# Kernel optimization log

Hardware: AMD Instinct MI355X
Metric: run time of the kernel (lower is better)

## Reference

```python
import jax, jax.numpy as jnp
import numpy as np

H, DH = 8, 64
DIM = 512
INNER = H * DH
GAMMA = 0.01
LAMBDA_REG = 0.001


def _ln(x, g, b, eps=1e-5):
    mu = x.mean(-1, keepdims=True)
    var = x.var(-1, keepdims=True)  # ddof=0, matches torch LayerNorm
    return (x - mu) / jnp.sqrt(var + eps) * g + b


def _proj(x, ln_g, ln_b, W):
    # LayerNorm -> Linear(no bias) -> split heads: [Q,N,DIM] -> [H,Q,N,DH]
    Q, N, _ = x.shape
    y = _ln(x, ln_g, ln_b) @ W
    return jnp.transpose(y.reshape(Q, N, H, DH), (2, 0, 1, 3))


def setup_inputs() -> dict:
    key = jax.random.key(0)
    ks = jax.random.split(key, 10)
    s = 0.02
    return {
        "q": jax.random.normal(ks[0], (16, 512, DIM), jnp.float32),
        "k": jax.random.normal(ks[1], (16, 512, DIM), jnp.float32),
        "v": jax.random.normal(ks[2], (16, 512, DIM), jnp.float32),
        "ln_g": jnp.ones((DIM,), jnp.float32),
        "ln_b": jnp.zeros((DIM,), jnp.float32),
        "W_in": jax.random.normal(ks[3], (DIM, INNER), jnp.float32) * s,
        "wp1_w": jax.random.normal(ks[4], (2 * DH, DH), jnp.float32) * s,
        "wp1_b": jnp.zeros((DH,), jnp.float32),
        "wpln_g": jnp.ones((DH,), jnp.float32),
        "wpln_b": jnp.zeros((DH,), jnp.float32),
        "wp2_w": jax.random.normal(ks[5], (DH, DH // 2), jnp.float32) * s,
        "wp2_b": jnp.zeros((DH // 2,), jnp.float32),
        "wp3_w": jax.random.normal(ks[6], (DH // 2, 3), jnp.float32) * s,
        "wp3_b": jnp.zeros((3,), jnp.float32),
        "temp": jnp.ones((1,), jnp.float32) * 5.0,
        "W_out": jax.random.normal(ks[7], (INNER, DIM), jnp.float32) * s,
        "b_out": jnp.zeros((DIM,), jnp.float32),
    }


def reference(q, k, v, ln_g, ln_b, W_in, wp1_w, wp1_b, wpln_g, wpln_b,
              wp2_w, wp2_b, wp3_w, wp3_b, temp, W_out, b_out):
    sg = jax.lax.stop_gradient
    std1 = lambda x: jnp.std(x, ddof=1)  # torch.std is unbiased

    f_q = _proj(q, ln_g, ln_b, W_in)  # [H,Q,N,DH]
    f_k = _proj(k, ln_g, ln_b, W_in)  # [H,Q,M,DH]
    f_v = _proj(v, ln_g, ln_b, W_in)
    m = f_k.shape[2]

    # --- cosine similarity component (cosine_distance + extra clamp) ---
    dots_raw = jnp.einsum('hqnd,hqmd->hqnm', f_q, f_k)
    n1 = jnp.linalg.norm(f_q, axis=-1, keepdims=True) + 1e-8          # [H,Q,N,1]
    n2 = jnp.linalg.norm(f_k, axis=-1, keepdims=True) + 1e-8          # [H,Q,M,1]
    cosine_sim = jnp.clip(dots_raw / (n1 * jnp.swapaxes(n2, -1, -2)), -0.99, 0.99)

    # --- regularized covariance component ---
    f_kc = f_k - f_k.mean(axis=2, keepdims=True)
    f_qc = f_q - f_q.mean(axis=-1, keepdims=True)
    cov = jnp.einsum('hqnd,hqmd->hqnm', f_qc, f_kc) / (DH ** 0.5 + 1e-8)
    cov = jnp.clip((LAMBDA_REG / max(m, 1)) * cov, -10.0, 10.0)

    # --- margin-based variance component (eval mode: adaptive_gamma == GAMMA) ---
    fqn = f_q / jnp.maximum(jnp.linalg.norm(f_q, axis=-1, keepdims=True), 1e-8)
    fkn = f_k / jnp.maximum(jnp.linalg.norm(f_k, axis=-1, keepdims=True), 1e-8)
    cs = jnp.clip(jnp.einsum('hqnd,hqmd->hqnm', fqn, fkn), -0.99, 0.99)
    margin = jnp.clip(GAMMA - cs, 0.0, 2.0)
    var_comp = jnp.broadcast_to(margin.mean(-1, keepdims=True), cs.shape)

    # --- dynamic weight predictor (dropouts identity in eval) ---
    qg = f_q.mean(axis=(1, 2))                 # [H,DH]
    kg = f_k.mean(axis=(1, 2))
    feats = jnp.concatenate([qg, kg], axis=-1)  # [H,2*DH]
    h1 = jax.nn.relu(_ln(feats @ wp1_w + wp1_b, wpln_g, wpln_b))
    h2 = jax.nn.relu(h1 @ wp2_w + wp2_b)
    logits = jax.nn.softmax(h2 @ wp3_w + wp3_b, axis=-1)  # softmax inside Sequential
    weights = jax.nn.softmax(logits / jnp.clip(temp, 0.1, 20.0), axis=-1)  # [H,3]
    cos_w = weights[:, 0].reshape(H, 1, 1, 1)
    cov_w = weights[:, 1].reshape(H, 1, 1, 1)
    var_w = weights[:, 2].reshape(H, 1, 1, 1)

    # --- global-std rescale + mix + adaptive temperature ---
    cos_s = cosine_sim / (sg(std1(cosine_sim)) + 1e-8)
    cov_s = cov / (sg(std1(cov)) + 1e-8) * 0.1
    var_s = var_comp / (sg(std1(var_comp)) + 1e-8) * 0.1
    dots = cos_w * cos_s + cov_w * cov_s + var_w * var_s
    attn_t = 1.0 + 0.5 * sg(std1(dots))
    dots = dots / jnp.clip(attn_t, 0.5, 5.0)

    out = jnp.einsum('hqnm,hqmd->hqnd', jax.nn.softmax(dots, axis=-1), f_v)
    out = jnp.transpose(out, (1, 2, 0, 3)).reshape(q.shape[0], q.shape[1], INNER)
    return out @ W_out + b_out
```

## Files before the change

kernel.cpp:

```cpp
#include <hip/hip_runtime.h>
#include <math.h>

#define NH 8
#define DHD 64
#define DMODEL 512
#define QB 16
#define SEQ 512
#define NROWS (QB*SEQ)
#define NHQ (NH*QB)
#define KCOV ((float)((0.001/512.0)/(8.0+1e-8)))

typedef __attribute__((ext_vector_type(8))) short short8;
typedef __attribute__((ext_vector_type(8))) unsigned short ushort8v;
typedef __attribute__((ext_vector_type(4))) unsigned short ushort4v;
typedef __attribute__((ext_vector_type(4))) float f32x4;

__device__ __forceinline__ float bf2f(unsigned short u){
  union { unsigned int i; float f; } c; c.i = ((unsigned int)u)<<16; return c.f;
}
__device__ __forceinline__ unsigned short f2bf(float f){
  union { float f; unsigned int i; } c; c.f = f;
  unsigned int u = c.i;
  u += 0x7fffu + ((u>>16)&1u);
  return (unsigned short)(u>>16);
}
__device__ __forceinline__ unsigned cvtpk(float a, float b){
  unsigned r; asm("v_cvt_pk_bf16_f32 %0, %1, %2" : "=v"(r) : "v"(a), "v"(b)); return r;
}
__device__ __forceinline__ float clampf(float x, float lo, float hi){ return fminf(fmaxf(x,lo),hi); }

__device__ __forceinline__ f32x4 MFMA(short8 a, short8 b, f32x4 c){
  return __builtin_amdgcn_mfma_f32_16x16x32_bf16(a, b, c, 0, 0, 0);
}
__device__ __forceinline__ short8 frag_ld(const unsigned short* T, int row, int rowbytes, int kbyte){
  int addr = row*rowbytes + (kbyte ^ ((row&7)<<4));
  return *reinterpret_cast<const short8*>(reinterpret_cast<const char*>(T) + addr);
}
__device__ __forceinline__ void tile_st16(unsigned short* T, int row, int rowbytes, int kbyte, ushort8v v){
  int addr = row*rowbytes + (kbyte ^ ((row&7)<<4));
  *reinterpret_cast<ushort8v*>(reinterpret_cast<char*>(T) + addr) = v;
}

__global__ void __launch_bounds__(256) prep_kernel(
    const float* __restrict__ xq, const float* __restrict__ xk, const float* __restrict__ xv,
    const float* __restrict__ ln_g, const float* __restrict__ ln_b,
    const float* __restrict__ Wi, const float* __restrict__ Wo,
    unsigned short* __restrict__ xln,
    unsigned short* __restrict__ WiT, unsigned short* __restrict__ WoT)
{
  __shared__ float T[64][68];
  int b = blockIdx.x, t = threadIdx.x;
  if (b < 6144){
    int which = b >> 11, rowblk = b & 2047;
    const float* src = which==0 ? xq : (which==1 ? xk : xv);
    int w = t >> 6, lane = t & 63;
    int row = rowblk*4 + w;
    const float* x = src + (size_t)row*DMODEL;
    float4 v1 = *reinterpret_cast<const float4*>(&x[lane*8]);
    float4 v2 = *reinterpret_cast<const float4*>(&x[lane*8+4]);
    float s  = v1.x+v1.y+v1.z+v1.w + v2.x+v2.y+v2.z+v2.w;
    float ss = v1.x*v1.x+v1.y*v1.y+v1.z*v1.z+v1.w*v1.w
             + v2.x*v2.x+v2.y*v2.y+v2.z*v2.z+v2.w*v2.w;
    #pragma unroll
    for (int m=32; m>0; m>>=1){ s += __shfl_xor(s,m,64); ss += __shfl_xor(ss,m,64); }
    float m_ = s*(1.0f/DMODEL);
    float var = ss*(1.0f/DMODEL) - m_*m_;
    float r_ = rsqrtf(var + 1e-5f);
    float4 g1 = *reinterpret_cast<const float4*>(&ln_g[lane*8]);
    float4 g2 = *reinterpret_cast<const float4*>(&ln_g[lane*8+4]);
    float4 b1 = *reinterpret_cast<const float4*>(&ln_b[lane*8]);
    float4 b2 = *reinterpret_cast<const float4*>(&ln_b[lane*8+4]);
    ushort8v o;
    o[0]=f2bf((v1.x-m_)*r_*g1.x + b1.x);
    o[1]=f2bf((v1.y-m_)*r_*g1.y + b1.y);
    o[2]=f2bf((v1.z-m_)*r_*g1.z + b1.z);
    o[3]=f2bf((v1.w-m_)*r_*g1.w + b1.w);
    o[4]=f2bf((v2.x-m_)*r_*g2.x + b2.x);
    o[5]=f2bf((v2.y-m_)*r_*g2.y + b2.y);
    o[6]=f2bf((v2.z-m_)*r_*g2.z + b2.z);
    o[7]=f2bf((v2.w-m_)*r_*g2.w + b2.w);
    *reinterpret_cast<ushort8v*>(&xln[((size_t)which*NROWS + row)*DMODEL + lane*8]) = o;
  } else {
    int wb = b - 6144;
    const float* src = (wb>=64) ? Wo : Wi;
    unsigned short* dst = (wb>=64) ? WoT : WiT;
    int rc = wb & 63;
    int r0 = (rc>>3)*64, c0 = (rc&7)*64;
    for (int it=0; it<4; ++it){
      int idx = it*256+t, row = idx>>4, q = idx&15;
      float4 v = *reinterpret_cast<const float4*>(&src[(size_t)(r0+row)*DMODEL + c0 + q*4]);
      T[row][q*4+0]=v.x; T[row][q*4+1]=v.y; T[row][q*4+2]=v.z; T[row][q*4+3]=v.w;
    }
    __syncthreads();
    for (int it=0; it<4; ++it){
      int idx = it*256+t, oc = idx>>4, q = idx&15;
      ushort4v o;
      o[0]=f2bf(T[q*4+0][oc]); o[1]=f2bf(T[q*4+1][oc]);
      o[2]=f2bf(T[q*4+2][oc]); o[3]=f2bf(T[q*4+3][oc]);
      *reinterpret_cast<ushort4v*>(&dst[(size_t)(c0+oc)*DMODEL + r0 + q*4]) = o;
    }
  }
}

__global__ void __launch_bounds__(256) proj_mfma_kernel(
    const unsigned short* __restrict__ xln,
    const unsigned short* __restrict__ WiT,
    unsigned short* __restrict__ fq, unsigned short* __restrict__ fk, unsigned short* __restrict__ fvT,
    float* __restrict__ aqA, float* __restrict__ i1qA,
    float* __restrict__ rskA, float* __restrict__ i1kA)
{
  int which = blockIdx.z;
  const unsigned short* src = xln + (size_t)which*NROWS*DMODEL;
  int r0 = blockIdx.x*128;
  int c0 = blockIdx.y*128;
  __shared__ unsigned short XT[128*64];
  __shared__ unsigned short WT[128*64];
  int t = threadIdx.x;
  int w=t>>6, lane=t&63, l16=lane&15, lh=lane>>4;
  f32x4 acc[4][4];
  #pragma unroll
  for(int i=0;i<4;i++){ for(int j=0;j<4;j++) acc[i][j]=(f32x4){0.f,0.f,0.f,0.f}; }
  for (int k0=0;k0<DMODEL;k0+=64){
    __syncthreads();
    for (int it=0; it<4; ++it){
      int idx=it*256+t, row=idx>>3, q=idx&7;
      ushort8v v = *reinterpret_cast<const ushort8v*>(&src[(size_t)(r0+row)*DMODEL + k0 + q*8]);
      tile_st16(XT, row, 128, q*16, v);
    }
    for (int it=0; it<4; ++it){
      int idx=it*256+t, row=idx>>3, q=idx&7;
      ushort8v v = *reinterpret_cast<const ushort8v*>(&WiT[(size_t)(c0+row)*DMODEL + k0 + q*8]);
      tile_st16(WT, row, 128, q*16, v);
    }
    __syncthreads();
    if (which<2){
      int dr=(w&1)*64, nc=(w>>1)*64;
      #pragma unroll
      for (int ks=0; ks<2; ++ks){
        int kb = lh*16 + ks*64;
        short8 a[4], b[4];
        #pragma unroll
        for (int i=0;i<4;i++) a[i] = frag_ld(WT, dr+i*16+l16, 128, kb);
        #pragma unroll
        for (int j=0;j<4;j++) b[j] = frag_ld(XT, nc+j*16+l16, 128, kb);
        #pragma unroll
        for (int i=0;i<4;i++){
          #pragma unroll
          for (int j=0;j<4;j++) acc[i][j]=MFMA(a[i],b[j],acc[i][j]);
        }
      }
    } else {
      int nr=(w>>1)*64, dc=(w&1)*64;
      #pragma unroll
      for (int ks=0; ks<2; ++ks){
        int kb = lh*16 + ks*64;
        short8 a[4], b[4];
        #pragma unroll
        for (int i=0;i<4;i++) a[i] = frag_ld(XT, nr+i*16+l16, 128, kb);
        #pragma unroll
        for (int j=0;j<4;j++) b[j] = frag_ld(WT, dc+j*16+l16, 128, kb);
        #pragma unroll
        for (int i=0;i<4;i++){
          #pragma unroll
          for (int j=0;j<4;j++) acc[i][j]=MFMA(a[i],b[j],acc[i][j]);
        }
      }
    }
  }
  if (which<2){
    unsigned short* dst = which ? fk : fq;
    int dr=(w&1)*64, nc=(w>>1)*64;
    #pragma unroll
    for (int i=0;i<4;i++){
      #pragma unroll
      for (int j=0;j<4;j++){
        int cl = c0 + dr + i*16 + lh*4;
        int ng = r0 + nc + j*16 + l16;
        int head = cl>>6, dd = cl&63;
        int hq = head*QB + (ng>>9);
        int n = ng&511;
        ushort4v o;
        o[0]=f2bf(acc[i][j][0]); o[1]=f2bf(acc[i][j][1]);
        o[2]=f2bf(acc[i][j][2]); o[3]=f2bf(acc[i][j][3]);
        *reinterpret_cast<ushort4v*>(&dst[((size_t)hq*SEQ+n)*DHD + dd]) = o;
      }
    }
    int head = (c0>>6) + (w&1);
    #pragma unroll
    for (int j=0;j<4;j++){
      float s=0.f, ss=0.f;
      #pragma unroll
      for (int i=0;i<4;i++){
        #pragma unroll
        for (int r=0;r<4;r++){ float x = acc[i][j][r]; s += x; ss = fmaf(x,x,ss); }
      }
      s += __shfl_xor(s,16,64); ss += __shfl_xor(ss,16,64);
      s += __shfl_xor(s,32,64); ss += __shfl_xor(ss,32,64);
      if (lh==0){
        int ng = r0 + nc + j*16 + l16;
        int hq = head*QB + (ng>>9);
        int n = ng&511;
        float nrm = sqrtf(ss);
        if (which==0){
          aqA[hq*SEQ+n]  = s*(1.0f/64.0f);
          i1qA[hq*SEQ+n] = 1.0f/(nrm+1e-8f);
        } else {
          rskA[hq*SEQ+n] = s;
          i1kA[hq*SEQ+n] = 1.0f/(nrm+1e-8f);
        }
      }
    }
  } else {
    int nr=(w>>1)*64, dc=(w&1)*64;
    #pragma unroll
    for (int i=0;i<4;i++){
      #pragma unroll
      for (int j=0;j<4;j++){
        int ngb = r0 + nr + i*16 + lh*4;
        int dg  = c0 + dc + j*16 + l16;
        int head = dg>>6, dd = dg&63;
        int hq = head*QB + (ngb>>9);
        int n = ngb&511;
        ushort4v o;
        o[0]=f2bf(acc[i][j][0]); o[1]=f2bf(acc[i][j][1]);
        o[2]=f2bf(acc[i][j][2]); o[3]=f2bf(acc[i][j][3]);
        *reinterpret_cast<ushort4v*>(&fvT[((size_t)hq*DHD+dd)*SEQ + n]) = o;
      }
    }
  }
}

__global__ void __launch_bounds__(256) colstat_kernel(
    const unsigned short* __restrict__ fq, const unsigned short* __restrict__ fk,
    float* __restrict__ qgp, float* __restrict__ kgp, float* __restrict__ c2A)
{
  int hq = blockIdx.x, isk = blockIdx.y;
  const unsigned short* F = (isk ? fk : fq) + (size_t)hq*SEQ*DHD;
  int t = threadIdx.x, g = t&15, rg = t>>4;
  float acc0=0.f, acc1=0.f, acc2=0.f, acc3=0.f;
  #pragma unroll 4
  for (int i=0;i<32;i++){
    int r = rg + 16*i;
    ushort4v v = *reinterpret_cast<const ushort4v*>(&F[(size_t)r*DHD + g*4]);
    acc0+=bf2f(v[0]); acc1+=bf2f(v[1]); acc2+=bf2f(v[2]); acc3+=bf2f(v[3]);
  }
  __shared__ float sh[16][68];
  sh[rg][g*4+0]=acc0; sh[rg][g*4+1]=acc1; sh[rg][g*4+2]=acc2; sh[rg][g*4+3]=acc3;
  __syncthreads();
  if (t<64){
    float s=0.f;
    #pragma unroll
    for (int r=0;r<16;r++) s += sh[r][t];
    if (isk){
      kgp[hq*64+t]=s;
      float c = s*(1.0f/512.0f);
      #pragma unroll
      for (int m=32;m>0;m>>=1) c += __shfl_xor(c,m,64);
      if (t==0) c2A[hq]=c;
    } else {
      qgp[hq*64+t]=s;
    }
  }
}

__global__ void __launch_bounds__(256) score_m1_kernel(
    const unsigned short* __restrict__ fq, const unsigned short* __restrict__ fk,
    const float* __restrict__ aqA, const float* __restrict__ i1qA,
    const float* __restrict__ rskA, const float* __restrict__ i1kA,
    const float* __restrict__ c2A, const float* __restrict__ kgp,
    float* __restrict__ c1A, float* __restrict__ rmaxcA, float* __restrict__ rmaxoA,
    float* __restrict__ momf, double* __restrict__ varp)
{
  int q_=blockIdx.x, h=blockIdx.y, strip=blockIdx.z;
  int hq=h*QB+q_, n0=strip*64;
  const unsigned short* Fq=fq+(size_t)hq*SEQ*DHD;
  const unsigned short* Fk=fk+(size_t)hq*SEQ*DHD;
  __shared__ unsigned short KT[128*64];
  __shared__ float rskL[512], i1kL[512];
  __shared__ float red[256];
  __shared__ double dred[256];
  int t=threadIdx.x, w=t>>6, lane=t&63, l16=lane&15, lh=lane>>4;
  int n = n0 + w*16 + l16;
  for (int i=t;i<512;i+=256){ rskL[i]=rskA[hq*SEQ+i]; i1kL[i]=i1kA[hq*SEQ+i]; }
  float c2v = c2A[hq];
  float aqv = aqA[hq*SEQ+n];
  float iq1 = i1qA[hq*SEQ+n];
  short8 qa[2];
  #pragma unroll
  for (int ks=0;ks<2;ks++)
    qa[ks] = *reinterpret_cast<const short8*>(&Fq[(size_t)n*DHD + ks*32 + lh*8]);
  float c1v = 0.f;
  #pragma unroll
  for (int ks=0;ks<2;ks++){
    const float* bkp = &kgp[hq*64 + ks*32 + lh*8];
    float4 b0 = *reinterpret_cast<const float4*>(bkp);
    float4 b1 = *reinterpret_cast<const float4*>(bkp+4);
    float bb[8] = {b0.x,b0.y,b0.z,b0.w,b1.x,b1.y,b1.z,b1.w};
    #pragma unroll
    for (int i=0;i<8;i++) c1v = fmaf(bf2f((unsigned short)qa[ks][i]), bb[i], c1v);
  }
  c1v *= (1.0f/512.0f);
  c1v += __shfl_xor(c1v,16,64);
  c1v += __shfl_xor(c1v,32,64);
  if (lane<16) c1A[hq*SEQ+n] = c1v;
  float c1x = KCOV*(c1v - aqv*c2v);
  float aqx = KCOV*aqv;
  float sc=0.f,sc2=0.f,so=0.f,so2=0.f,sco=0.f;
  float rc=0.f, ro=0.f, rm=0.f, rmc=-1e30f, rmo=-1e30f;
  for (int mc=0;mc<4;mc++){
    int m0=mc*128;
    __syncthreads();
    for (int it=0;it<4;++it){
      int idx=it*256+t, row=idx>>3, qc=idx&7;
      ushort8v vv = *reinterpret_cast<const ushort8v*>(&Fk[(size_t)(m0+row)*DHD + qc*8]);
      tile_st16(KT,row,128,qc*16,vv);
    }
    __syncthreads();
    #pragma unroll
    for (int mh=0;mh<2;mh++){
      int mb = mh*64;
      f32x4 acc[4];
      #pragma unroll
      for (int mf=0;mf<4;mf++) acc[mf]=(f32x4){0.f,0.f,0.f,0.f};
      #pragma unroll
      for (int mf=0;mf<4;mf++){
        #pragma unroll
        for (int ks=0;ks<2;ks++){
          short8 kf = frag_ld(KT, mb+mf*16+l16, 128, lh*16+ks*64);
          acc[mf] = MFMA(kf, qa[ks], acc[mf]);
        }
      }
      #pragma unroll
      for (int mf=0;mf<4;mf++){
        int ml = m0 + mb + mf*16 + lh*4;
        float4 rsk4 = *reinterpret_cast<const float4*>(&rskL[ml]);
        float4 i1k4 = *reinterpret_cast<const float4*>(&i1kL[ml]);
        float rk[4]={rsk4.x,rsk4.y,rsk4.z,rsk4.w};
        float ik[4]={i1k4.x,i1k4.y,i1k4.z,i1k4.w};
        #pragma unroll
        for (int r=0;r<4;r++){
          float S = acc[mf][r];
          float cosv = clampf(S*iq1*ik[r], -0.99f, 0.99f);
          float u = fmaf(KCOV, S, -c1x);
          float covv = fmaf(-aqx, rk[r], u);
          covv = clampf(covv, -10.0f, 10.0f);
          float marg = clampf(0.01f - cosv, 0.0f, 2.0f);
          sc += cosv; sc2 = fmaf(cosv,cosv,sc2);
          so += covv; so2 = fmaf(covv,covv,so2);
          sco = fmaf(cosv,covv,sco);
          rc += cosv; ro += covv; rm += marg;
          rmc = fmaxf(rmc, cosv); rmo = fmaxf(rmo, covv);
        }
      }
    }
  }
  rc += __shfl_xor(rc,16,64); rc += __shfl_xor(rc,32,64);
  ro += __shfl_xor(ro,16,64); ro += __shfl_xor(ro,32,64);
  rm += __shfl_xor(rm,16,64); rm += __shfl_xor(rm,32,64);
  rmc = fmaxf(rmc, __shfl_xor(rmc,16,64)); rmc = fmaxf(rmc, __shfl_xor(rmc,32,64));
  rmo = fmaxf(rmo, __shfl_xor(rmo,16,64)); rmo = fmaxf(rmo, __shfl_xor(rmo,32,64));
  if (lane<16){
    rmaxcA[hq*SEQ+n] = rmc;
    rmaxoA[hq*SEQ+n] = rmo;
  }
  double vm=0.0, vm2=0.0, vmc=0.0, vmo=0.0;
  if (lane<16){
    float mm = rm*(1.0f/512.0f);
    vm  = (double)mm;
    vm2 = (double)mm*(double)mm;
    vmc = (double)mm*(double)rc;
    vmo = (double)mm*(double)ro;
  }
  float fs[5]={sc,sc2,so,so2,sco};
  for (int c=0;c<5;c++){
    __syncthreads();
    red[t]=fs[c]; __syncthreads();
    for (int o=128;o>0;o>>=1){ if (t<o) red[t]+=red[t+o]; __syncthreads(); }
    if (t==0) momf[(size_t)(hq*8+strip)*5 + c] = red[0];
  }
  double ds[4]={vm,vm2,vmc,vmo};
  for (int c=0;c<4;c++){
    __syncthreads();
    dred[t]=ds[c]; __syncthreads();
    for (int o=128;o>0;o>>=1){ if (t<o) dred[t]+=dred[t+o]; __syncthreads(); }
    if (t==0) varp[(size_t)(hq*8+strip)*4 + c] = dred[0];
  }
}

__global__ void __launch_bounds__(256) finalize_kernel(
    const float* __restrict__ qgp, const float* __restrict__ kgp,
    const float* __restrict__ wp1w, const float* __restrict__ wp1b,
    const float* __restrict__ wplg, const float* __restrict__ wplb,
    const float* __restrict__ wp2w, const float* __restrict__ wp2b,
    const float* __restrict__ wp3w, const float* __restrict__ wp3b,
    const float* __restrict__ temp,
    const float* __restrict__ momf, const double* __restrict__ varp,
    float* __restrict__ params)
{
  int t = threadIdx.x;
  __shared__ float feats[8][128];
  __shared__ float h1s[8][64];
  __shared__ float h2s[8][32];
  __shared__ float wts[8][3];
  __shared__ double Sh[8][9];
  for (int idx=t; idx<512; idx+=256){
    int h = idx>>6, d = idx&63;
    float s1=0, s2=0;
    for (int qq=0; qq<QB; qq++){ s1 += qgp[(h*QB+qq)*64+d]; s2 += kgp[(h*QB+qq)*64+d]; }
    feats[h][d]    = s1*(1.0f/8192.0f);
    feats[h][64+d] = s2*(1.0f/8192.0f);
  }
  __syncthreads();
  int w = t>>6, j = t&63;
  for (int pp=0; pp<2; pp++){
    int h = w + pp*4;
    float acc = wp1b[j];
    for (int k=0;k<128;k++) acc += feats[h][k]*wp1w[k*64+j];
    float s=acc, s2=acc*acc;
    #pragma unroll
    for (int m=32;m>0;m>>=1){ s+=__shfl_xor(s,m,64); s2+=__shfl_xor(s2,m,64); }
    float mean = s*(1.0f/64.0f);
    float var  = s2*(1.0f/64.0f) - mean*mean;
    float xh = (acc-mean)*rsqrtf(var+1e-5f)*wplg[j] + wplb[j];
    h1s[h][j] = fmaxf(xh, 0.0f);
  }
  __syncthreads();
  {
    int h = t>>5, j2 = t&31;
    float acc = wp2b[j2];
    for (int k=0;k<64;k++) acc += h1s[h][k]*wp2w[k*32+j2];
    h2s[h][j2] = fmaxf(acc, 0.0f);
  }
  __syncthreads();
  if (t<8){
    int h = t;
    float z[3] = {wp3b[0], wp3b[1], wp3b[2]};
    for (int k=0;k<32;k++){
      float hv = h2s[h][k];
      z[0]+=hv*wp3w[k*3]; z[1]+=hv*wp3w[k*3+1]; z[2]+=hv*wp3w[k*3+2];
    }
    float mx = fmaxf(z[0], fmaxf(z[1], z[2]));
    float e0=expf(z[0]-mx), e1=expf(z[1]-mx), e2=expf(z[2]-mx);
    float inv = 1.0f/(e0+e1+e2);
    float l0=e0*inv, l1=e1*inv, l2=e2*inv;
    float tv = temp[0]; tv = fminf(fmaxf(tv, 0.1f), 20.0f);
    float y0=l0/tv, y1=l1/tv, y2=l2/tv;
    float mx2 = fmaxf(y0, fmaxf(y1, y2));
    float f0=expf(y0-mx2), f1=expf(y1-mx2), f2=expf(y2-mx2);
    float inv2 = 1.0f/(f0+f1+f2);
    wts[h][0]=f0*inv2; wts[h][1]=f1*inv2; wts[h][2]=f2*inv2;
  }
  __syncthreads();
  if (t<40){
    int h = t/5, c = t%5;
    double s = 0;
    for (int e=0; e<128; e++) s += (double)momf[(size_t)(h*128+e)*5 + c];
    Sh[h][c] = s;
  }
  __syncthreads();
  if (t<32){
    int h = t>>2, c = t&3;
    double s = 0;
    for (int e=0; e<128; e++) s += varp[(size_t)(h*128+e)*4 + c];
    Sh[h][5+c] = s;
  }
  __syncthreads();
  if (t==0){
    const double Ntot = 33554432.0;
    double T1c=0,T2c=0,T1o=0,T2o=0,T1v=0,T2v=0;
    for (int h=0;h<8;h++){
      T1c+=Sh[h][0]; T2c+=Sh[h][1]; T1o+=Sh[h][2]; T2o+=Sh[h][3];
      T1v+=512.0*Sh[h][5]; T2v+=512.0*Sh[h][6];
    }
    double stdc = sqrt(fmax((T2c - T1c*T1c/Ntot)/(Ntot-1.0), 0.0));
    double stdo = sqrt(fmax((T2o - T1o*T1o/Ntot)/(Ntot-1.0), 0.0));
    double stdv = sqrt(fmax((T2v - T1v*T1v/Ntot)/(Ntot-1.0), 0.0));
    double ah[8], bh[8];
    double Sd1=0, Sd2=0;
    for (int h=0;h<8;h++){
      double a = (double)wts[h][0]/(stdc+1e-8);
      double b = (double)wts[h][1]*0.1/(stdo+1e-8);
      double c = (double)wts[h][2]*0.1/(stdv+1e-8);
      ah[h]=a; bh[h]=b;
      Sd1 += a*Sh[h][0] + b*Sh[h][2] + c*512.0*Sh[h][5];
      Sd2 += a*a*Sh[h][1] + b*b*Sh[h][3] + c*c*512.0*Sh[h][6]
           + 2.0*a*b*Sh[h][4] + 2.0*a*c*Sh[h][7] + 2.0*b*c*Sh[h][8];
    }
    double stdd = sqrt(fmax((Sd2 - Sd1*Sd1/Ntot)/(Ntot-1.0), 0.0));
    double att = 1.0 + 0.5*stdd;
    att = fmin(fmax(att, 0.5), 5.0);
    double scale = 1.0/att;
    for (int h=0;h<8;h++){
      params[h*2+0] = (float)(scale*ah[h]);
      params[h*2+1] = (float)(scale*bh[h]);
    }
  }
}

__global__ void __launch_bounds__(256) attn_m2_kernel(
    const unsigned short* __restrict__ fq, const unsigned short* __restrict__ fk,
    const unsigned short* __restrict__ fvT,
    const float* __restrict__ aqA, const float* __restrict__ c1A, const float* __restrict__ i1qA,
    const float* __restrict__ rskA, const float* __restrict__ i1kA,
    const float* __restrict__ c2A, const float* __restrict__ params,
    const float* __restrict__ rmaxcA, const float* __restrict__ rmaxoA,
    unsigned short* __restrict__ attn_bf)
{
  int q_=blockIdx.x, h=blockIdx.y, strip=blockIdx.z;
  int hq=h*QB+q_, n0=strip*64;
  const unsigned short* Fq=fq+(size_t)hq*SEQ*DHD;
  const unsigned short* Fk=fk+(size_t)hq*SEQ*DHD;
  const unsigned short* FvT=fvT+(size_t)hq*DHD*SEQ;
  __shared__ unsigned short KT[128*64];
  __shared__ unsigned short VT[64*128];
  __shared__ unsigned short P[64*64];
  __shared__ float rskL[512], i1kL[512];
  int t=threadIdx.x, w=t>>6, lane=t&63, l16=lane&15, lh=lane>>4;
  int n = n0 + w*16 + l16;
  for (int i=t;i<512;i+=256){ rskL[i]=rskA[hq*SEQ+i]; i1kL[i]=i1kA[hq*SEQ+i]; }
  float c2v=c2A[hq];
  float pa=params[h*2], pb=params[h*2+1];
  float aqv = aqA[hq*SEQ+n];
  float c1v = c1A[hq*SEQ+n];
  float iq1 = i1qA[hq*SEQ+n];
  float rmc = rmaxcA[hq*SEQ+n];
  float rmo = rmaxoA[hq*SEQ+n];
  float pbk = pb*KCOV;
  float ra  = pa*iq1;
  float bndc = 0.99f*pa;
  float rowc = -pbk*(c1v - aqv*c2v);
  float r3   = pbk*aqv;
  float Mrow = fmaf(pa, rmc, pb*rmo);
  short8 qa[2];
  #pragma unroll
  for (int ks=0;ks<2;ks++)
    qa[ks] = *reinterpret_cast<const short8*>(&Fq[(size_t)n*DHD + ks*32 + lh*8]);
  short8 ones;
  #pragma unroll
  for (int i=0;i<8;i++) ones[i] = (short)0x3F80;
  f32x4 accO[4];
  #pragma unroll
  for (int j=0;j<4;j++) accO[j]=(f32x4){0.f,0.f,0.f,0.f};
  f32x4 den = (f32x4){0.f,0.f,0.f,0.f};
  int prow = w*16 + l16;
  for (int mc=0;mc<4;mc++){
    int m0=mc*128;
    __syncthreads();
    for (int it=0;it<4;++it){
      int idx=it*256+t, row=idx>>3, qc=idx&7;
      ushort8v vv = *reinterpret_cast<const ushort8v*>(&Fk[(size_t)(m0+row)*DHD + qc*8]);
      tile_st16(KT,row,128,qc*16,vv);
    }
    for (int it=0;it<4;++it){
      int idx=it*256+t, dd=idx>>4, c=idx&15;
      ushort8v vv=*reinterpret_cast<const ushort8v*>(&FvT[(size_t)dd*SEQ + m0 + c*8]);
      tile_st16(VT, dd, 256, c*16, vv);
    }
    __syncthreads();
    #pragma unroll
    for (int mh=0;mh<2;mh++){
      int mb = mh*64;
      f32x4 acc[4];
      #pragma unroll
      for (int mf=0;mf<4;mf++) acc[mf]=(f32x4){0.f,0.f,0.f,0.f};
      #pragma unroll
      for (int mf=0;mf<4;mf++){
        #pragma unroll
        for (int ks=0;ks<2;ks++){
          short8 kf = frag_ld(KT, mb+mf*16+l16, 128, lh*16+ks*64);
          acc[mf] = MFMA(kf, qa[ks], acc[mf]);
        }
      }
      #pragma unroll
      for (int mf=0;mf<4;mf++){
        int ml = m0 + mb + mf*16 + lh*4;
        float4 rsk4 = *reinterpret_cast<const float4*>(&rskL[ml]);
        float4 i1k4 = *reinterpret_cast<const float4*>(&i1kL[ml]);
        float rk[4]={rsk4.x,rsk4.y,rsk4.z,rsk4.w};
        float ik[4]={i1k4.x,i1k4.y,i1k4.z,i1k4.w};
        #pragma unroll
        for (int r=0;r<4;r++){
          float S = acc[mf][r];
          float tt = S*ra; tt *= ik[r];
          float cc = clampf(tt, -bndc, bndc);
          float u = fmaf(pbk, S, rowc);
          float lin = fmaf(-r3, rk[r], u);
          acc[mf][r] = __expf(cc + lin - Mrow);
        }
        unsigned lo = cvtpk(acc[mf][0], acc[mf][1]);
        unsigned hi = cvtpk(acc[mf][2], acc[mf][3]);
        int pbyte = (mf*32 + lh*8) ^ ((prow&7)<<4);
        *reinterpret_cast<uint2*>(reinterpret_cast<char*>(P) + prow*128 + pbyte)
          = make_uint2(lo, hi);
      }
      #pragma unroll
      for (int ks=0;ks<2;ks++){
        short8 pfrag = frag_ld(P, prow, 128, lh*16 + ks*64);
        #pragma unroll
        for (int dcf=0;dcf<4;dcf++){
          short8 vb = frag_ld(VT, dcf*16+l16, 256, mb*2 + ks*64 + lh*16);
          accO[dcf] = MFMA(pfrag, vb, accO[dcf]);
        }
        den = MFMA(pfrag, ones, den);
      }
    }
  }
  f32x4 invD;
  #pragma unroll
  for (int r=0;r<4;r++) invD[r] = 1.0f/den[r];
  __syncthreads();
  #pragma unroll
  for (int dcf=0;dcf<4;dcf++){
    #pragma unroll
    for (int r=0;r<4;r++){
      int row = w*16 + lh*4 + r;
      int col = dcf*16 + l16;
      int addr = row*128 + ((col*2) ^ ((row&7)<<4));
      *reinterpret_cast<unsigned short*>(reinterpret_cast<char*>(P) + addr)
        = f2bf(accO[dcf][r]*invD[r]);
    }
  }
  __syncthreads();
  for (int it=0; it<2; ++it){
    int idx = it*256 + t;
    int row = idx>>3, c = idx&7;
    int addr = row*128 + ((c*16) ^ ((row&7)<<4));
    ushort8v vv = *reinterpret_cast<ushort8v*>(reinterpret_cast<char*>(P) + addr);
    *reinterpret_cast<ushort8v*>(
      &attn_bf[(size_t)(q_*SEQ + n0 + row)*DMODEL + h*DHD + c*8]) = vv;
  }
}

__global__ void __launch_bounds__(256) out_mfma_kernel(
    const unsigned short* __restrict__ attn_bf, const unsigned short* __restrict__ WoT,
    const float* __restrict__ bias, float* __restrict__ out)
{
  int r0=blockIdx.x*128;
  int c0=blockIdx.y*128;
  __shared__ unsigned short AT[128*64];
  __shared__ unsigned short WT[128*64];
  int t=threadIdx.x, w=t>>6, lane=t&63, l16=lane&15, lh=lane>>4;
  f32x4 acc[4][4];
  #pragma unroll
  for(int i=0;i<4;i++){ for(int j=0;j<4;j++) acc[i][j]=(f32x4){0.f,0.f,0.f,0.f}; }
  for (int k0=0;k0<DMODEL;k0+=64){
    __syncthreads();
    for (int it=0; it<4; ++it){
      int idx=it*256+t, row=idx>>3, q=idx&7;
      ushort8v v = *reinterpret_cast<const ushort8v*>(&attn_bf[(size_t)(r0+row)*DMODEL + k0 + q*8]);
      tile_st16(AT, row, 128, q*16, v);
    }
    for (int it=0; it<4; ++it){
      int idx=it*256+t, row=idx>>3, q=idx&7;
      ushort8v v = *reinterpret_cast<const ushort8v*>(&WoT[(size_t)(c0+row)*DMODEL + k0 + q*8]);
      tile_st16(WT, row, 128, q*16, v);
    }
    __syncthreads();
    int nr=(w&1)*64, mr=(w>>1)*64;
    #pragma unroll
    for (int ks=0; ks<2; ++ks){
      int kb = lh*16 + ks*64;
      short8 a[4], b[4];
      #pragma unroll
      for (int i=0;i<4;i++) a[i] = frag_ld(WT, nr+i*16+l16, 128, kb);
      #pragma unroll
      for (int j=0;j<4;j++) b[j] = frag_ld(AT, mr+j*16+l16, 128, kb);
      #pragma unroll
      for (int i=0;i<4;i++){
        #pragma unroll
        for (int j=0;j<4;j++) acc[i][j]=MFMA(a[i],b[j],acc[i][j]);
      }
    }
  }
  #pragma unroll
  for (int i=0;i<4;i++){
    int nb = c0+(w&1)*64+i*16+lh*4;
    float4 b4 = *reinterpret_cast<const float4*>(&bias[nb]);
    #pragma unroll
    for (int j=0;j<4;j++){
      int mg = r0+(w>>1)*64+j*16+l16;
      f32x4 o = acc[i][j];
      o[0]+=b4.x; o[1]+=b4.y; o[2]+=b4.z; o[3]+=b4.w;
      *reinterpret_cast<f32x4*>(&out[(size_t)mg*DMODEL + nb]) = o;
    }
  }
}

extern "C" void kernel_launch(void* const* d_in, const int* in_sizes, int n_in,
                              void* d_out, int out_size, void* d_ws, size_t ws_size,
                              hipStream_t stream)
{
  (void)in_sizes; (void)n_in; (void)out_size; (void)ws_size;
  const float* q     = (const float*)d_in[0];
  const float* k     = (const float*)d_in[1];
  const float* v     = (const float*)d_in[2];
  const float* ln_g  = (const float*)d_in[3];
  const float* ln_b  = (const float*)d_in[4];
  const float* W_in  = (const float*)d_in[5];
  const float* wp1w  = (const float*)d_in[6];
  const float* wp1b  = (const float*)d_in[7];
  const float* wplg  = (const float*)d_in[8];
  const float* wplb  = (const float*)d_in[9];
  const float* wp2w  = (const float*)d_in[10];
  const float* wp2b  = (const float*)d_in[11];
  const float* wp3w  = (const float*)d_in[12];
  const float* wp3b  = (const float*)d_in[13];
  const float* temp  = (const float*)d_in[14];
  const float* W_out = (const float*)d_in[15];
  const float* b_out = (const float*)d_in[16];
  float* out = (float*)d_out;

  char* wsb = (char*)d_ws;
  size_t off = 0;
  auto alloc = [&](size_t bytes)->char*{
    char* p = wsb + off; off += (bytes + 255) & ~(size_t)255; return p;
  };
  unsigned short* xln    = (unsigned short*)alloc((size_t)3*NROWS*DMODEL*2);
  unsigned short* fq_b   = (unsigned short*)alloc((size_t)NHQ*SEQ*DHD*2);
  unsigned short* fk_b   = (unsigned short*)alloc((size_t)NHQ*SEQ*DHD*2);
  unsigned short* fvT_b  = (unsigned short*)alloc((size_t)NHQ*SEQ*DHD*2);
  unsigned short* attn_b = (unsigned short*)alloc((size_t)NROWS*DMODEL*2);
  unsigned short* WiT    = (unsigned short*)alloc((size_t)DMODEL*DMODEL*2);
  unsigned short* WoT    = (unsigned short*)alloc((size_t)DMODEL*DMODEL*2);
  float* aqA    = (float*)alloc(NHQ*SEQ*4);
  float* c1A    = (float*)alloc(NHQ*SEQ*4);
  float* i1qA   = (float*)alloc(NHQ*SEQ*4);
  float* rskA   = (float*)alloc(NHQ*SEQ*4);
  float* i1kA   = (float*)alloc(NHQ*SEQ*4);
  float* rmaxcA = (float*)alloc(NHQ*SEQ*4);
  float* rmaxoA = (float*)alloc(NHQ*SEQ*4);
  float* c2A    = (float*)alloc(NHQ*4);
  float* qgp    = (float*)alloc(NHQ*64*4);
  float* kgp    = (float*)alloc(NHQ*64*4);
  float* momf   = (float*)alloc((size_t)NHQ*8*5*4);
  double* varp  = (double*)alloc((size_t)NHQ*8*4*8);
  float* params = (float*)alloc(64);

  prep_kernel<<<6272, 256, 0, stream>>>(q, k, v, ln_g, ln_b, W_in, W_out, xln, WiT, WoT);
  proj_mfma_kernel<<<dim3(64,4,3), 256, 0, stream>>>(xln, WiT, fq_b, fk_b, fvT_b,
                                                     aqA, i1qA, rskA, i1kA);
  colstat_kernel<<<dim3(NHQ, 2), 256, 0, stream>>>(fq_b, fk_b, qgp, kgp, c2A);
  score_m1_kernel<<<dim3(QB, NH, 8), 256, 0, stream>>>(fq_b, fk_b, aqA, i1qA, rskA, i1kA,
                                                       c2A, kgp, c1A, rmaxcA, rmaxoA, momf, varp);
  finalize_kernel<<<1, 256, 0, stream>>>(qgp, kgp, wp1w, wp1b, wplg, wplb, wp2w, wp2b,
                                         wp3w, wp3b, temp, momf, varp, params);
  attn_m2_kernel<<<dim3(QB, NH, 8), 256, 0, stream>>>(fq_b, fk_b, fvT_b, aqA, c1A, i1qA,
                                                      rskA, i1kA, c2A, params, rmaxcA, rmaxoA, attn_b);
  out_mfma_kernel<<<dim3(64,4), 256, 0, stream>>>(attn_b, WoT, b_out, out);
}
```

Baseline: 163.2 us.

## Prefetch next global tiles into registers before MFMA compute in four kernels

```diff
diff --git a/kernel.cpp b/kernel.cpp
--- a/kernel.cpp
+++ b/kernel.cpp
@@ -117,22 +117,31 @@
   __shared__ unsigned short WT[128*64];
   int t = threadIdx.x;
   int w=t>>6, lane=t&63, l16=lane&15, lh=lane>>4;
+  int srow = t>>3, sq = t&7;
   f32x4 acc[4][4];
   #pragma unroll
   for(int i=0;i<4;i++){ for(int j=0;j<4;j++) acc[i][j]=(f32x4){0.f,0.f,0.f,0.f}; }
+  ushort8v xr[4], wr[4];
+  #pragma unroll
+  for (int it=0; it<4; ++it){
+    xr[it] = *reinterpret_cast<const ushort8v*>(&src[(size_t)(r0+srow+it*32)*DMODEL + sq*8]);
+    wr[it] = *reinterpret_cast<const ushort8v*>(&WiT[(size_t)(c0+srow+it*32)*DMODEL + sq*8]);
+  }
   for (int k0=0;k0<DMODEL;k0+=64){
     __syncthreads();
+    #pragma unroll
     for (int it=0; it<4; ++it){
-      int idx=it*256+t, row=idx>>3, q=idx&7;
-      ushort8v v = *reinterpret_cast<const ushort8v*>(&src[(size_t)(r0+row)*DMODEL + k0 + q*8]);
-      tile_st16(XT, row, 128, q*16, v);
-    }
-    for (int it=0; it<4; ++it){
-      int idx=it*256+t, row=idx>>3, q=idx&7;
-      ushort8v v = *reinterpret_cast<const ushort8v*>(&WiT[(size_t)(c0+row)*DMODEL + k0 + q*8]);
-      tile_st16(WT, row, 128, q*16, v);
-    }
-    __syncthreads();
+      tile_st16(XT, srow+it*32, 128, sq*16, xr[it]);
+      tile_st16(WT, srow+it*32, 128, sq*16, wr[it]);
+    }
+    __syncthreads();
+    if (k0+64 < DMODEL){
+      #pragma unroll
+      for (int it=0; it<4; ++it){
+        xr[it] = *reinterpret_cast<const ushort8v*>(&src[(size_t)(r0+srow+it*32)*DMODEL + k0+64 + sq*8]);
+        wr[it] = *reinterpret_cast<const ushort8v*>(&WiT[(size_t)(c0+srow+it*32)*DMODEL + k0+64 + sq*8]);
+      }
+    }
     if (which<2){
       int dr=(w&1)*64, nc=(w>>1)*64;
       #pragma unroll
@@ -281,6 +290,7 @@
   __shared__ double dred[256];
   int t=threadIdx.x, w=t>>6, lane=t&63, l16=lane&15, lh=lane>>4;
   int n = n0 + w*16 + l16;
+  int srow = t>>3, sq = t&7;
   for (int i=t;i<512;i+=256){ rskL[i]=rskA[hq*SEQ+i]; i1kL[i]=i1kA[hq*SEQ+i]; }
   float c2v = c2A[hq];
   float aqv = aqA[hq*SEQ+n];
@@ -305,17 +315,24 @@
   if (lane<16) c1A[hq*SEQ+n] = c1v;
   float c1x = KCOV*(c1v - aqv*c2v);
   float aqx = KCOV*aqv;
+  ushort8v kr[4];
+  #pragma unroll
+  for (int it=0;it<4;++it)
+    kr[it] = *reinterpret_cast<const ushort8v*>(&Fk[(size_t)(srow+it*32)*DHD + sq*8]);
   float sc=0.f,sc2=0.f,so=0.f,so2=0.f,sco=0.f;
   float rc=0.f, ro=0.f, rm=0.f, rmc=-1e30f, rmo=-1e30f;
   for (int mc=0;mc<4;mc++){
     int m0=mc*128;
     __syncthreads();
-    for (int it=0;it<4;++it){
-      int idx=it*256+t, row=idx>>3, qc=idx&7;
-      ushort8v vv = *reinterpret_cast<const ushort8v*>(&Fk[(size_t)(m0+row)*DHD + qc*8]);
-      tile_st16(KT,row,128,qc*16,vv);
-    }
-    __syncthreads();
+    #pragma unroll
+    for (int it=0;it<4;++it)
+      tile_st16(KT, srow+it*32, 128, sq*16, kr[it]);
+    __syncthreads();
+    if (mc<3){
+      #pragma unroll
+      for (int it=0;it<4;++it)
+        kr[it] = *reinterpret_cast<const ushort8v*>(&Fk[(size_t)(m0+128+srow+it*32)*DHD + sq*8]);
+    }
     #pragma unroll
     for (int mh=0;mh<2;mh++){
       int mb = mh*64;
@@ -517,6 +534,8 @@
   __shared__ float rskL[512], i1kL[512];
   int t=threadIdx.x, w=t>>6, lane=t&63, l16=lane&15, lh=lane>>4;
   int n = n0 + w*16 + l16;
+  int srow = t>>3, sq = t&7;
+  int vd = t>>4, vc = t&15;
   for (int i=t;i<512;i+=256){ rskL[i]=rskA[hq*SEQ+i]; i1kL[i]=i1kA[hq*SEQ+i]; }
   float c2v=c2A[hq];
   float pa=params[h*2], pb=params[h*2+1];
@@ -543,20 +562,28 @@
   for (int j=0;j<4;j++) accO[j]=(f32x4){0.f,0.f,0.f,0.f};
   f32x4 den = (f32x4){0.f,0.f,0.f,0.f};
   int prow = w*16 + l16;
+  ushort8v kr[4], vr[4];
+  #pragma unroll
+  for (int it=0;it<4;++it){
+    kr[it] = *reinterpret_cast<const ushort8v*>(&Fk[(size_t)(srow+it*32)*DHD + sq*8]);
+    vr[it] = *reinterpret_cast<const ushort8v*>(&FvT[(size_t)(vd+it*16)*SEQ + vc*8]);
+  }
   for (int mc=0;mc<4;mc++){
     int m0=mc*128;
     __syncthreads();
+    #pragma unroll
     for (int it=0;it<4;++it){
-      int idx=it*256+t, row=idx>>3, qc=idx&7;
-      ushort8v vv = *reinterpret_cast<const ushort8v*>(&Fk[(size_t)(m0+row)*DHD + qc*8]);
-      tile_st16(KT,row,128,qc*16,vv);
-    }
-    for (int it=0;it<4;++it){
-      int idx=it*256+t, dd=idx>>4, c=idx&15;
-      ushort8v vv=*reinterpret_cast<const ushort8v*>(&FvT[(size_t)dd*SEQ + m0 + c*8]);
-      tile_st16(VT, dd, 256, c*16, vv);
-    }
-    __syncthreads();
+      tile_st16(KT, srow+it*32, 128, sq*16, kr[it]);
+      tile_st16(VT, vd+it*16, 256, vc*16, vr[it]);
+    }
+    __syncthreads();
+    if (mc<3){
+      #pragma unroll
+      for (int it=0;it<4;++it){
+        kr[it] = *reinterpret_cast<const ushort8v*>(&Fk[(size_t)(m0+128+srow+it*32)*DHD + sq*8]);
+        vr[it] = *reinterpret_cast<const ushort8v*>(&FvT[(size_t)(vd+it*16)*SEQ + m0+128 + vc*8]);
+      }
+    }
     #pragma unroll
     for (int mh=0;mh<2;mh++){
       int mb = mh*64;
@@ -640,22 +667,31 @@
   __shared__ unsigned short AT[128*64];
   __shared__ unsigned short WT[128*64];
   int t=threadIdx.x, w=t>>6, lane=t&63, l16=lane&15, lh=lane>>4;
+  int srow = t>>3, sq = t&7;
   f32x4 acc[4][4];
   #pragma unroll
   for(int i=0;i<4;i++){ for(int j=0;j<4;j++) acc[i][j]=(f32x4){0.f,0.f,0.f,0.f}; }
+  ushort8v ar[4], wr[4];
+  #pragma unroll
+  for (int it=0; it<4; ++it){
+    ar[it] = *reinterpret_cast<const ushort8v*>(&attn_bf[(size_t)(r0+srow+it*32)*DMODEL + sq*8]);
+    wr[it] = *reinterpret_cast<const ushort8v*>(&WoT[(size_t)(c0+srow+it*32)*DMODEL + sq*8]);
+  }
   for (int k0=0;k0<DMODEL;k0+=64){
     __syncthreads();
+    #pragma unroll
     for (int it=0; it<4; ++it){
-      int idx=it*256+t, row=idx>>3, q=idx&7;
-      ushort8v v = *reinterpret_cast<const ushort8v*>(&attn_bf[(size_t)(r0+row)*DMODEL + k0 + q*8]);
-      tile_st16(AT, row, 128, q*16, v);
-    }
-    for (int it=0; it<4; ++it){
-      int idx=it*256+t, row=idx>>3, q=idx&7;
-      ushort8v v = *reinterpret_cast<const ushort8v*>(&WoT[(size_t)(c0+row)*DMODEL + k0 + q*8]);
-      tile_st16(WT, row, 128, q*16, v);
-    }
-    __syncthreads();
+      tile_st16(AT, srow+it*32, 128, sq*16, ar[it]);
+      tile_st16(WT, srow+it*32, 128, sq*16, wr[it]);
+    }
+    __syncthreads();
+    if (k0+64 < DMODEL){
+      #pragma unroll
+      for (int it=0; it<4; ++it){
+        ar[it] = *reinterpret_cast<const ushort8v*>(&attn_bf[(size_t)(r0+srow+it*32)*DMODEL + k0+64 + sq*8]);
+        wr[it] = *reinterpret_cast<const ushort8v*>(&WoT[(size_t)(c0+srow+it*32)*DMODEL + k0+64 + sq*8]);
+      }
+    }
     int nr=(w&1)*64, mr=(w>>1)*64;
     #pragma unroll
     for (int ks=0; ks<2; ++ks){
```

Result: faster. 139.3 us, median of 4 (-14.6%).
